# Optimization experiments

Measured on AMD Instinct MI355X. Metric: run time of the kernel, lower is better.

The kernel has to match this reference:

```python
import math
import jax, jax.numpy as jnp
import numpy as np

B, S, F, I, K, L, C = 2, 2048, 512, 1024, 3, 2, 256
BETA = 0.99                 # momentumnet_beta
INIT_SCALE = L ** -0.5      # per-cell output scale
PI = math.pi


def setup_inputs() -> dict:
    key = jax.random.key(0)
    ks = jax.random.split(key, 8)
    inp = jax.random.randint(ks[0], (B, S), 0, C)
    tgt = jax.random.randint(ks[1], (B, S), 0, C)
    emb = jax.random.normal(ks[2], (C, 2 * F), jnp.float32) * 0.02
    w0s = jax.random.normal(ks[3], (L, 3, I, F, 1), jnp.float32) * (F ** -0.5)
    w1s = jax.random.normal(ks[4], (L, 3, I, I, K), jnp.float32) * ((I * K) ** -0.5)
    w2s = jax.random.normal(ks[5], (L, 3, F, I, 1), jnp.float32) * (I ** -0.5)
    out_w = jax.random.normal(ks[6], (C, 2 * F, 1), jnp.float32) * ((2 * F) ** -0.5)
    out_b = jax.random.normal(ks[7], (C,), jnp.float32) * 0.02
    return {"inp": inp, "tgt": tgt, "emb": emb, "w0s": w0s, "w1s": w1s,
            "w2s": w2s, "out_w": out_w, "out_b": out_b}


def causal_conv(x, w):
    # x: [B, Cin, S], w: [Cout, Cin, k]; left-pad k-1 (matches torch pad+(k-1,0)+conv1d)
    k = w.shape[-1]
    return jax.lax.conv_general_dilated(x, w, (1,), [(k - 1, 0)],
                                        dimension_numbers=("NCH", "OIH", "NCH"))


def feed_forward(x, w0, w1, w2):
    x = jax.nn.relu(causal_conv(x, w0))
    x = jax.nn.relu(causal_conv(x, w1))
    return causal_conv(x, w2)


def norm(x):
    # mean-subtract + RMS-style L2 norm over channel dim (dim 1)
    x = x - x.mean(1, keepdims=True)
    return x / (jnp.linalg.norm(x, axis=1, keepdims=True) * (x.shape[1] ** -0.5) + 1e-5)


def _feature_embd():
    f = jnp.arange(F, dtype=jnp.float32)[:, None] + 1.0
    additive = f % 2.0
    f = (f - additive) / 2.0
    f = f * (8.0 / F) - math.log(C / (2.0 * PI))
    return jnp.exp(f) + additive * PI  # [F, 1]


def _forward(inp, tgt, emb, w0s, w1s, w2s, out_w, out_b):
    fe = _feature_embd()
    divisor = (jnp.arange(S, dtype=jnp.float32) + 1.0)[None, None, :]  # [1,1,S]
    x = emb[inp].transpose(0, 2, 1)         # [B, 2F, S]
    a, b = x[:, :F], x[:, F:]               # reversible streams [B, F, S]
    for l in range(L):
        h = b + fe                          # training-path positional embedding
        d = feed_forward(h, w0s[l, 0], w1s[l, 0], w2s[l, 0])
        sc = feed_forward(h, w0s[l, 1], w1s[l, 1], w2s[l, 1])
        sh = feed_forward(h, w0s[l, 2], w1s[l, 2], w2s[l, 2])
        cum = jnp.cumsum(d, axis=1)         # cumsum over feature dim (dim 1, as in source)
        cell = norm(cum / divisor * sc + sh) * INIT_SCALE
        c = BETA * a + (1.0 - BETA) * cell  # momentum coupling forward
        a, b = c, b + c                     # Identity layer with additive coupling
    streams = jnp.concatenate([a, b], axis=1)        # [B, 2F, S]
    logits = causal_conv(streams, out_w) + out_b[None, :, None]  # [B, C, S]
    logp = jax.nn.log_softmax(logits, axis=1)
    nll = -jnp.take_along_axis(logp, tgt[:, None, :], axis=1)[:, 0, :]
    return nll.mean()                       # torch cross_entropy (mean reduction)


def reference(inp, tgt, emb, w0s, w1s, w2s, out_w, out_b):
    return _forward(inp, tgt, emb, w0s, w1s, w2s, out_w, out_b)
```

## Files before the change

kernel.cpp:

```cpp
#include <hip/hip_runtime.h>

#define S_ 2048
#define F_ 512
#define I_ 1024
#define C_ 256

typedef float f4 __attribute__((ext_vector_type(4)));
typedef __bf16 bf8 __attribute__((ext_vector_type(8)));
typedef __bf16 bf4 __attribute__((ext_vector_type(4)));
typedef int i4v __attribute__((ext_vector_type(4)));
typedef int i8v __attribute__((ext_vector_type(8)));
typedef unsigned char u8;

__device__ __forceinline__ void gload_lds16(const void* g, void* l) {
  __builtin_amdgcn_global_load_lds(
      (const __attribute__((address_space(1))) void*)g,
      (__attribute__((address_space(3))) void*)l, 16, 0, 0);
}

__device__ __forceinline__ float fe_val(int f) {
  const float PI_F = 3.14159265358979323846f;
  float additive = (f & 1) ? 0.0f : 1.0f;
  float fv = ((float)(f + 1) - additive) * 0.5f;
  fv = fv * (8.0f / (float)F_) - logf((float)C_ / (2.0f * PI_F));
  return expf(fv) + additive * PI_F;
}

template <int KW, bool RELU, int OUT, int NTILE, int KD, int LDB>
__global__ __launch_bounds__(256) void gemm_f8(
    const u8* __restrict__ Ab, const u8* __restrict__ Bb, void* __restrict__ Cb,
    const u8* __restrict__ zpage, int M, int PZ, long sAp, long sBp, long sBb,
    long sCz) {
  constexpr int NF = NTILE / 32;
  constexpr int NIT = KD / 128;
  constexpr int AK = KW * KD;
  constexpr int BP = NTILE / 32;
  __shared__ u8 Asm[128 * 128];
  __shared__ u8 Bsm[NTILE * 128];
  const int tid = threadIdx.x;
  const int z = blockIdx.z;
  const int p = z % PZ;
  const int bb = z / PZ;
  const u8* A = Ab + (long)p * sAp;
  const u8* B = Bb + (long)bb * sBb + (long)p * sBp;
  const int m0 = blockIdx.y * 128;
  const int n0 = blockIdx.x * NTILE;
  const int lane = tid & 63;
  const int wave = tid >> 6;
  const int wr = wave >> 1;
  const int wc = wave & 1;
  const int l15 = lane & 15;
  const int quad = lane >> 4;
  const int cr = tid >> 3;
  const int csw = (((tid & 7) ^ (cr & 7)) << 4);
  const int off0 = (((2 * quad) ^ (l15 & 7)) << 4);
  const int off1 = (((2 * quad + 1) ^ (l15 & 7)) << 4);
  f4 acc[4][NF] = {};

  for (int t = 0; t < KW; ++t) {
    const u8* pA = A + (long)t * KD;
    const u8* pB[BP];
#pragma unroll
    for (int g = 0; g < BP; ++g) {
      const int rg = n0 + g * 32 + cr + ((KW == 3) ? (t - 2) : 0);
      pB[g] = (KW == 3 && rg < 0) ? (zpage + csw) : (B + (long)rg * LDB + csw);
    }
#pragma unroll 1
    for (int it = 0; it < NIT; ++it) {
      const int kb = it * 128;
#pragma unroll
      for (int g = 0; g < 4; ++g)
        gload_lds16(pA + (long)(m0 + g * 32 + cr) * AK + kb + csw,
                    Asm + g * 4096 + wave * 1024);
#pragma unroll
      for (int g = 0; g < BP; ++g)
        gload_lds16(pB[g] + kb, Bsm + g * 4096 + wave * 1024);
      __syncthreads();
      i8v af[4], bfr[NF];
#pragma unroll
      for (int mt = 0; mt < 4; ++mt) {
        const u8* rp = Asm + (wr * 64 + mt * 16 + l15) * 128;
        const i4v lo = *(const i4v*)(rp + off0);
        const i4v hi = *(const i4v*)(rp + off1);
        af[mt][0] = lo[0]; af[mt][1] = lo[1]; af[mt][2] = lo[2]; af[mt][3] = lo[3];
        af[mt][4] = hi[0]; af[mt][5] = hi[1]; af[mt][6] = hi[2]; af[mt][7] = hi[3];
      }
#pragma unroll
      for (int nt = 0; nt < NF; ++nt) {
        const u8* rp = Bsm + (wc * (NTILE / 2) + nt * 16 + l15) * 128;
        const i4v lo = *(const i4v*)(rp + off0);
        const i4v hi = *(const i4v*)(rp + off1);
        bfr[nt][0] = lo[0]; bfr[nt][1] = lo[1]; bfr[nt][2] = lo[2]; bfr[nt][3] = lo[3];
        bfr[nt][4] = hi[0]; bfr[nt][5] = hi[1]; bfr[nt][6] = hi[2]; bfr[nt][7] = hi[3];
      }
#pragma unroll
      for (int mt = 0; mt < 4; ++mt)
#pragma unroll
        for (int nt = 0; nt < NF; ++nt)
          acc[mt][nt] = __builtin_amdgcn_mfma_scale_f32_16x16x128_f8f6f4(
              af[mt], bfr[nt], acc[mt][nt], 0, 0, 0, 0x7F7F7F7F, 0, 0x7F7F7F7F);
      __syncthreads();
    }
  }
#pragma unroll
  for (int mt = 0; mt < 4; ++mt) {
    const int m = m0 + wr * 64 + mt * 16 + quad * 4;
#pragma unroll
    for (int nt = 0; nt < NF; ++nt) {
      const int n = n0 + wc * (NTILE / 2) + nt * 16 + l15;
      f4 v = acc[mt][nt];
#pragma unroll
      for (int q = 0; q < 4; ++q) {
        v[q] *= 0.015625f;
        if (RELU) v[q] = fmaxf(v[q], 0.0f);
      }
      if (OUT == 2) {
        int r = __builtin_amdgcn_cvt_pk_fp8_f32(v[0], v[1], 0, false);
        r = __builtin_amdgcn_cvt_pk_fp8_f32(v[2], v[3], r, true);
        *(int*)((u8*)Cb + (long)z * sCz + (long)n * M + m) = r;
      } else {
        *(f4*)((float*)Cb + (long)z * sCz + (long)n * M + m) = v;
      }
    }
  }
}

__device__ __forceinline__ void cvt4(const float* __restrict__ s,
                                     __bf16* __restrict__ d, long T) {
  const long i = T * 4;
  const float4 v = *(const float4*)(s + i);
  bf4 o;
  o[0] = (__bf16)v.x;
  o[1] = (__bf16)v.y;
  o[2] = (__bf16)v.z;
  o[3] = (__bf16)v.w;
  *(bf4*)(d + i) = o;
}

__device__ __forceinline__ void cvt4f8(const float* __restrict__ s,
                                       u8* __restrict__ d, long T) {
  const long i = T * 4;
  const float4 v = *(const float4*)(s + i);
  int r = __builtin_amdgcn_cvt_pk_fp8_f32(v.x * 64.0f, v.y * 64.0f, 0, false);
  r = __builtin_amdgcn_cvt_pk_fp8_f32(v.z * 64.0f, v.w * 64.0f, r, true);
  *(int*)(d + i) = r;
}

__device__ __forceinline__ int pk4f8(float a, float b, float c, float d) {
  int r = __builtin_amdgcn_cvt_pk_fp8_f32(a, b, 0, false);
  return __builtin_amdgcn_cvt_pk_fp8_f32(c, d, r, true);
}

__global__ void k_prep(const float* __restrict__ w0, const float* __restrict__ w2,
                       const float* __restrict__ ow, const float* __restrict__ w1,
                       u8* __restrict__ W0f8, u8* __restrict__ W2f8,
                       __bf16* __restrict__ OWc, u8* __restrict__ W1f8) {
  long T = (long)blockIdx.x * 256 + threadIdx.x;
  if (T < 786432L) {
    cvt4f8(w0, W0f8, T);
    return;
  }
  T -= 786432L;
  if (T < 786432L) {
    cvt4f8(w2, W2f8, T);
    return;
  }
  T -= 786432L;
  if (T < 65536L) {
    cvt4(ow, OWc, T);
    return;
  }
  T -= 65536L;
  const long j4 = T & 255;
  const long r3 = T >> 8;
  const float* src = w1 + r3 * 3072 + j4 * 12;
  const float4 v0 = *(const float4*)src;
  const float4 v1 = *(const float4*)(src + 4);
  const float4 v2 = *(const float4*)(src + 8);
  u8* dst = W1f8 + r3 * 3072 + j4 * 4;
  *(int*)(dst) = pk4f8(v0.x * 64.f, v0.w * 64.f, v1.z * 64.f, v2.y * 64.f);
  *(int*)(dst + 1024) = pk4f8(v0.y * 64.f, v1.x * 64.f, v1.w * 64.f, v2.z * 64.f);
  *(int*)(dst + 2048) = pk4f8(v0.z * 64.f, v1.y * 64.f, v2.x * 64.f, v2.w * 64.f);
}

__global__ __launch_bounds__(64) void k_embed(const int* __restrict__ inp,
                                              const float* __restrict__ emb,
                                              float* __restrict__ a_st,
                                              float* __restrict__ b_st,
                                              u8* __restrict__ h) {
  const int col = blockIdx.x;
  const int lane = threadIdx.x;
  const int f0 = lane * 8;
  const float* e = emb + (long)inp[col] * (2 * F_);
  const float4 a0 = *(const float4*)(e + f0);
  const float4 a1 = *(const float4*)(e + f0 + 4);
  const float4 b0 = *(const float4*)(e + F_ + f0);
  const float4 b1 = *(const float4*)(e + F_ + f0 + 4);
  *(float4*)(a_st + (long)col * F_ + f0) = a0;
  *(float4*)(a_st + (long)col * F_ + f0 + 4) = a1;
  *(float4*)(b_st + (long)col * F_ + f0) = b0;
  *(float4*)(b_st + (long)col * F_ + f0 + 4) = b1;
  const float bb[8] = {b0.x, b0.y, b0.z, b0.w, b1.x, b1.y, b1.z, b1.w};
  float hv[8];
#pragma unroll
  for (int q = 0; q < 8; ++q) hv[q] = bb[q] + fe_val(f0 + q);
  const int lo = pk4f8(hv[0], hv[1], hv[2], hv[3]);
  const int hi = pk4f8(hv[4], hv[5], hv[6], hv[7]);
  *(int2*)(h + (long)col * F_ + f0) = {lo, hi};
}

__global__ __launch_bounds__(64) void k_cell(const float* __restrict__ Y3,
                                             float* __restrict__ a_st,
                                             float* __restrict__ b_st,
                                             void* __restrict__ outp,
                                             int last) {
  const int col = blockIdx.x;
  const int s = col & (S_ - 1);
  const int b = col >> 11;
  const int lane = threadIdx.x;
  const int f0 = lane * 8;
  const float* d = Y3 + ((long)(3 * b + 0) * S_ + s) * F_ + f0;
  const float* sc = Y3 + ((long)(3 * b + 1) * S_ + s) * F_ + f0;
  const float* sh = Y3 + ((long)(3 * b + 2) * S_ + s) * F_ + f0;
  float* ap = a_st + (long)col * F_ + f0;
  float* bp = b_st + (long)col * F_ + f0;
  const float inv_div = 1.0f / (float)(s + 1);

  const float4 d0 = *(const float4*)d;
  const float4 d1 = *(const float4*)(d + 4);
  const float4 sc0 = *(const float4*)sc;
  const float4 sc1 = *(const float4*)(sc + 4);
  const float4 sh0 = *(const float4*)sh;
  const float4 sh1 = *(const float4*)(sh + 4);

  float c[8];
  c[0] = d0.x;
  c[1] = c[0] + d0.y;
  c[2] = c[1] + d0.z;
  c[3] = c[2] + d0.w;
  c[4] = c[3] + d1.x;
  c[5] = c[4] + d1.y;
  c[6] = c[5] + d1.z;
  c[7] = c[6] + d1.w;
  const float tot = c[7];
  float scan = tot;
#pragma unroll
  for (int off = 1; off < 64; off <<= 1) {
    float nb = __shfl_up(scan, off);
    if (lane >= off) scan += nb;
  }
  const float base = scan - tot;

  float v[8];
  v[0] = (base + c[0]) * inv_div * sc0.x + sh0.x;
  v[1] = (base + c[1]) * inv_div * sc0.y + sh0.y;
  v[2] = (base + c[2]) * inv_div * sc0.z + sh0.z;
  v[3] = (base + c[3]) * inv_div * sc0.w + sh0.w;
  v[4] = (base + c[4]) * inv_div * sc1.x + sh1.x;
  v[5] = (base + c[5]) * inv_div * sc1.y + sh1.y;
  v[6] = (base + c[6]) * inv_div * sc1.z + sh1.z;
  v[7] = (base + c[7]) * inv_div * sc1.w + sh1.w;

  float sum = 0.f, ssq = 0.f;
#pragma unroll
  for (int q = 0; q < 8; ++q) {
    sum += v[q];
    ssq += v[q] * v[q];
  }
#pragma unroll
  for (int off = 1; off < 64; off <<= 1) {
    sum += __shfl_xor(sum, off);
    ssq += __shfl_xor(ssq, off);
  }
  const float mean = sum * (1.0f / (float)F_);
  const float nsq = fmaxf(ssq - (float)F_ * mean * mean, 0.0f);
  const float denom = sqrtf(nsq) * 0.04419417382415922f + 1e-5f;
  const float isc = 0.7071067811865476f / denom;

  const float4 av0 = *(const float4*)ap;
  const float4 av1 = *(const float4*)(ap + 4);
  const float4 bv0 = *(const float4*)bp;
  const float4 bv1 = *(const float4*)(bp + 4);
  float an[8], bn[8];
  const float ai[8] = {av0.x, av0.y, av0.z, av0.w, av1.x, av1.y, av1.z, av1.w};
  const float bi[8] = {bv0.x, bv0.y, bv0.z, bv0.w, bv1.x, bv1.y, bv1.z, bv1.w};
#pragma unroll
  for (int q = 0; q < 8; ++q) {
    const float cell = (v[q] - mean) * isc;
    an[q] = 0.99f * ai[q] + 0.01f * cell;
    bn[q] = bi[q] + an[q];
  }
  *(float4*)ap = {an[0], an[1], an[2], an[3]};
  *(float4*)(ap + 4) = {an[4], an[5], an[6], an[7]};
  *(float4*)bp = {bn[0], bn[1], bn[2], bn[3]};
  *(float4*)(bp + 4) = {bn[4], bn[5], bn[6], bn[7]};
  if (!last) {
    float hv[8];
#pragma unroll
    for (int q = 0; q < 8; ++q) hv[q] = bn[q] + fe_val(f0 + q);
    const int lo = pk4f8(hv[0], hv[1], hv[2], hv[3]);
    const int hi = pk4f8(hv[4], hv[5], hv[6], hv[7]);
    *(int2*)((u8*)outp + (long)col * F_ + f0) = {lo, hi};
  } else {
    bf8 oa, ob;
#pragma unroll
    for (int q = 0; q < 8; ++q) {
      oa[q] = (__bf16)an[q];
      ob[q] = (__bf16)bn[q];
    }
    *(bf8*)((__bf16*)outp + (long)col * (2 * F_) + f0) = oa;
    *(bf8*)((__bf16*)outp + (long)col * (2 * F_) + F_ + f0) = ob;
  }
}

__global__ __launch_bounds__(256) void k_logits_nll(
    const __bf16* __restrict__ A, const __bf16* __restrict__ Bb,
    const float* __restrict__ outb, const int* __restrict__ tgt,
    float* __restrict__ acc) {
  __shared__ __bf16 As[256 * 32];
  __shared__ __bf16 Bs[32 * 32];
  __shared__ float lsm[32 * 256];
  const int tid = threadIdx.x;
  const int b = blockIdx.y;
  const int n0 = blockIdx.x * 32;
  const __bf16* Bt = Bb + (long)b * (S_ * 2 * F_) + (long)n0 * (2 * F_);
  const int lane = tid & 63;
  const int wave = tid >> 6;
  const int l15 = lane & 15;
  const int quad = lane >> 4;
  const int cr = tid >> 2;
  const int csw = (((tid & 3) ^ ((cr >> 1) & 3)) << 3);
  const int roff = ((quad ^ ((l15 >> 1) & 3)) << 3);
  f4 av[4][2] = {};
  for (int k0 = 0; k0 < 2 * F_; k0 += 32) {
#pragma unroll
    for (int i = 0; i < 4; ++i)
      gload_lds16(A + (long)(i * 64 + cr) * (2 * F_) + (k0 + csw),
                  As + ((i * 256 + (wave << 6)) << 3));
    if (wave < 2)
      gload_lds16(Bt + (long)cr * (2 * F_) + (k0 + csw),
                  Bs + ((wave << 6) << 3));
    __syncthreads();
    bf8 af[4], bfr[2];
#pragma unroll
    for (int mt = 0; mt < 4; ++mt)
      af[mt] = *(const bf8*)(As + (wave * 64 + mt * 16 + l15) * 32 + roff);
#pragma unroll
    for (int nt = 0; nt < 2; ++nt)
      bfr[nt] = *(const bf8*)(Bs + (nt * 16 + l15) * 32 + roff);
#pragma unroll
    for (int mt = 0; mt < 4; ++mt)
#pragma unroll
      for (int nt = 0; nt < 2; ++nt)
        av[mt][nt] = __builtin_amdgcn_mfma_f32_16x16x32_bf16(af[mt], bfr[nt],
                                                             av[mt][nt], 0, 0, 0);
    __syncthreads();
  }
#pragma unroll
  for (int mt = 0; mt < 4; ++mt) {
    const int m = wave * 64 + mt * 16 + quad * 4;
#pragma unroll
    for (int nt = 0; nt < 2; ++nt) {
      const int pp = nt * 16 + l15;
      *(f4*)(lsm + pp * C_ + m) = av[mt][nt];
    }
  }
  __syncthreads();
  const float4 bv = *(const float4*)(outb + lane * 4);
  float wsum = 0.f;
  for (int i = 0; i < 8; ++i) {
    const int pp = wave * 8 + i;
    const f4 lv = *(const f4*)(lsm + pp * C_ + lane * 4);
    const float x0 = lv[0] + bv.x, x1 = lv[1] + bv.y, x2 = lv[2] + bv.z,
                x3 = lv[3] + bv.w;
    float mx = fmaxf(fmaxf(x0, x1), fmaxf(x2, x3));
#pragma unroll
    for (int off = 1; off < 64; off <<= 1) mx = fmaxf(mx, __shfl_xor(mx, off));
    float ss = expf(x0 - mx) + expf(x1 - mx) + expf(x2 - mx) + expf(x3 - mx);
#pragma unroll
    for (int off = 1; off < 64; off <<= 1) ss += __shfl_xor(ss, off);
    if (lane == 0) {
      const int t = tgt[b * S_ + n0 + pp];
      wsum += mx + logf(ss) - (lsm[pp * C_ + t] + outb[t]);
    }
  }
  if (lane == 0) atomicAdd(acc, wsum);
}

__global__ void k_final(const float* __restrict__ acc, float* __restrict__ out) {
  out[0] = acc[0] * (1.0f / 4096.0f);
}

extern "C" void kernel_launch(void* const* d_in, const int* in_sizes, int n_in,
                              void* d_out, int out_size, void* d_ws,
                              size_t ws_size, hipStream_t stream) {
  const int* inp = (const int*)d_in[0];
  const int* tgt = (const int*)d_in[1];
  const float* emb = (const float*)d_in[2];
  const float* w0s = (const float*)d_in[3];
  const float* w1s = (const float*)d_in[4];
  const float* w2s = (const float*)d_in[5];
  const float* out_w = (const float*)d_in[6];
  const float* out_b = (const float*)d_in[7];

  char* ws = (char*)d_ws;
  float* acc = (float*)(ws + 0);
  u8* zp = (u8*)(ws + 256);
  float* a_st = (float*)(ws + 4096);
  float* b_st = (float*)(ws + 8392704L);
  u8* h = (u8*)(ws + 16781312L);
  u8* Y1f8 = (u8*)(ws + 20975616L);
  u8* Y2f8 = (u8*)(ws + 46141440L);
  float* Y3 = (float*)(ws + 71307264L);
  u8* W1f8 = (u8*)(ws + 96473088L);
  __bf16* streams = (__bf16*)(ws + 134221824L);
  u8* W0f8 = (u8*)(ws + 146804736L);
  u8* W2f8 = (u8*)(ws + 153096192L);
  __bf16* OWc = (__bf16*)(ws + 159387648L);

  hipMemsetAsync(ws, 0, 4096, stream);
  k_prep<<<12544, 256, 0, stream>>>(w0s, w2s, out_w, w1s, W0f8, W2f8, OWc, W1f8);
  k_embed<<<4096, 64, 0, stream>>>(inp, emb, a_st, b_st, h);

  for (int l = 0; l < 2; ++l) {
    gemm_f8<1, true, 2, 128, 512, 512><<<dim3(16, 24, 2), 256, 0, stream>>>(
        W0f8 + (long)l * 1572864L, h, Y1f8, zp, 3072, 1, 0L, 0L, 1048576L,
        6291456L);
    gemm_f8<3, true, 2, 128, 1024, 3072><<<dim3(16, 8, 6), 256, 0, stream>>>(
        W1f8 + (long)l * 9437184L, Y1f8, Y2f8, zp, 1024, 3, 3145728L, 1024L,
        6291456L, 2097152L);
    gemm_f8<1, false, 0, 64, 1024, 1024><<<dim3(32, 4, 6), 256, 0, stream>>>(
        W2f8 + (long)l * 1572864L, Y2f8, Y3, zp, 512, 3, 524288L, 2097152L,
        6291456L, 1048576L);
    k_cell<<<4096, 64, 0, stream>>>(Y3, a_st, b_st,
                                    (l == 0) ? (void*)h : (void*)streams,
                                    (l == 1) ? 1 : 0);
  }

  k_logits_nll<<<dim3(64, 2), 256, 0, stream>>>(OWc, streams, out_b, tgt, acc);
  k_final<<<1, 1, 0, stream>>>(acc, (float*)d_out);
}
```

Baseline: 354.8 us.

## Double-buffer LDS tiles in fp8 GEMM to overlap loads with MFMA

Converts the fp8 GEMM main loop to use two LDS buffers, issuing the next k-step's global-to-LDS loads before computing on the current buffer. The aim is to hide global load latency behind MFMA work, where before each step loaded, synchronised and then computed serially. This doubles LDS usage per block, which can lower occupancy, and it requires an even k-step count, enforced by a static_assert.

```diff
diff --git a/kernel.cpp b/kernel.cpp
--- a/kernel.cpp
+++ b/kernel.cpp
@@ -35,8 +35,10 @@
   constexpr int NIT = KD / 128;
   constexpr int AK = KW * KD;
   constexpr int BP = NTILE / 32;
-  __shared__ u8 Asm[128 * 128];
-  __shared__ u8 Bsm[NTILE * 128];
+  constexpr int NSTEP = KW * NIT;
+  static_assert(NSTEP % 2 == 0, "even k-step count required");
+  __shared__ u8 Asm[2][128 * 128];
+  __shared__ u8 Bsm[2][NTILE * 128];
   const int tid = threadIdx.x;
   const int z = blockIdx.z;
   const int p = z % PZ;
@@ -57,51 +59,60 @@
   const int off1 = (((2 * quad + 1) ^ (l15 & 7)) << 4);
   f4 acc[4][NF] = {};
 
-  for (int t = 0; t < KW; ++t) {
-    const u8* pA = A + (long)t * KD;
-    const u8* pB[BP];
+  auto stage = [&](int ks, int buf) {
+    const int t = ks / NIT;
+    const int kb = (ks % NIT) * 128;
+    const u8* pA = A + (long)t * KD + kb + csw + (long)(m0 + cr) * AK;
+#pragma unroll
+    for (int g = 0; g < 4; ++g)
+      gload_lds16(pA + (long)(g * 32) * AK, Asm[buf] + g * 4096 + wave * 1024);
 #pragma unroll
     for (int g = 0; g < BP; ++g) {
       const int rg = n0 + g * 32 + cr + ((KW == 3) ? (t - 2) : 0);
-      pB[g] = (KW == 3 && rg < 0) ? (zpage + csw) : (B + (long)rg * LDB + csw);
-    }
+      const u8* pB = (KW == 3 && rg < 0) ? (zpage + kb + csw)
+                                         : (B + (long)rg * LDB + kb + csw);
+      gload_lds16(pB, Bsm[buf] + g * 4096 + wave * 1024);
+    }
+  };
+
+  auto compute = [&](int buf) {
+    i8v af[4], bfr[NF];
+#pragma unroll
+    for (int mt = 0; mt < 4; ++mt) {
+      const u8* rp = Asm[buf] + (wr * 64 + mt * 16 + l15) * 128;
+      const i4v lo = *(const i4v*)(rp + off0);
+      const i4v hi = *(const i4v*)(rp + off1);
+      af[mt][0] = lo[0]; af[mt][1] = lo[1]; af[mt][2] = lo[2]; af[mt][3] = lo[3];
+      af[mt][4] = hi[0]; af[mt][5] = hi[1]; af[mt][6] = hi[2]; af[mt][7] = hi[3];
+    }
+#pragma unroll
+    for (int nt = 0; nt < NF; ++nt) {
+      const u8* rp = Bsm[buf] + (wc * (NTILE / 2) + nt * 16 + l15) * 128;
+      const i4v lo = *(const i4v*)(rp + off0);
+      const i4v hi = *(const i4v*)(rp + off1);
+      bfr[nt][0] = lo[0]; bfr[nt][1] = lo[1]; bfr[nt][2] = lo[2]; bfr[nt][3] = lo[3];
+      bfr[nt][4] = hi[0]; bfr[nt][5] = hi[1]; bfr[nt][6] = hi[2]; bfr[nt][7] = hi[3];
+    }
+#pragma unroll
+    for (int mt = 0; mt < 4; ++mt)
+#pragma unroll
+      for (int nt = 0; nt < NF; ++nt)
+        acc[mt][nt] = __builtin_amdgcn_mfma_scale_f32_16x16x128_f8f6f4(
+            af[mt], bfr[nt], acc[mt][nt], 0, 0, 0, 0x7F7F7F7F, 0, 0x7F7F7F7F);
+  };
+
+  stage(0, 0);
+  __syncthreads();
 #pragma unroll 1
-    for (int it = 0; it < NIT; ++it) {
-      const int kb = it * 128;
-#pragma unroll
-      for (int g = 0; g < 4; ++g)
-        gload_lds16(pA + (long)(m0 + g * 32 + cr) * AK + kb + csw,
-                    Asm + g * 4096 + wave * 1024);
-#pragma unroll
-      for (int g = 0; g < BP; ++g)
-        gload_lds16(pB[g] + kb, Bsm + g * 4096 + wave * 1024);
-      __syncthreads();
-      i8v af[4], bfr[NF];
-#pragma unroll
-      for (int mt = 0; mt < 4; ++mt) {
-        const u8* rp = Asm + (wr * 64 + mt * 16 + l15) * 128;
-        const i4v lo = *(const i4v*)(rp + off0);
-        const i4v hi = *(const i4v*)(rp + off1);
-        af[mt][0] = lo[0]; af[mt][1] = lo[1]; af[mt][2] = lo[2]; af[mt][3] = lo[3];
-        af[mt][4] = hi[0]; af[mt][5] = hi[1]; af[mt][6] = hi[2]; af[mt][7] = hi[3];
-      }
-#pragma unroll
-      for (int nt = 0; nt < NF; ++nt) {
-        const u8* rp = Bsm + (wc * (NTILE / 2) + nt * 16 + l15) * 128;
-        const i4v lo = *(const i4v*)(rp + off0);
-        const i4v hi = *(const i4v*)(rp + off1);
-        bfr[nt][0] = lo[0]; bfr[nt][1] = lo[1]; bfr[nt][2] = lo[2]; bfr[nt][3] = lo[3];
-        bfr[nt][4] = hi[0]; bfr[nt][5] = hi[1]; bfr[nt][6] = hi[2]; bfr[nt][7] = hi[3];
-      }
-#pragma unroll
-      for (int mt = 0; mt < 4; ++mt)
-#pragma unroll
-        for (int nt = 0; nt < NF; ++nt)
-          acc[mt][nt] = __builtin_amdgcn_mfma_scale_f32_16x16x128_f8f6f4(
-              af[mt], bfr[nt], acc[mt][nt], 0, 0, 0, 0x7F7F7F7F, 0, 0x7F7F7F7F);
-      __syncthreads();
-    }
-  }
+  for (int ks = 0; ks < NSTEP; ks += 2) {
+    stage(ks + 1, 1);
+    compute(0);
+    __syncthreads();
+    if (ks + 2 < NSTEP) stage(ks + 2, 0);
+    compute(1);
+    __syncthreads();
+  }
+
 #pragma unroll
   for (int mt = 0; mt < 4; ++mt) {
     const int m = m0 + wr * 64 + mt * 16 + quad * 4;
```

New measurement: 376.1 us. +6.0%, slower.
